# Kernel tuning notes

Measured on AMD Instinct MI355X. Metric: run time of the kernel, lower is better.

The kernel has to match this reference:

```python
import jax, jax.numpy as jnp
import numpy as np

B, E, H = 32768, 512, 512


def setup_inputs() -> dict:
    key = jax.random.key(0)
    ks = jax.random.split(key, 7)
    s_e = 1.0 / np.sqrt(E)
    s_h = 1.0 / np.sqrt(H)
    return {
        "input": jax.random.normal(ks[0], (B, E), jnp.float32),
        "h0": jax.random.normal(ks[1], (B, H), jnp.float32),
        "c0": jax.random.normal(ks[2], (B, H), jnp.float32),
        # stacked weights, gate order [i, f, o, g]
        "W_x": jax.random.uniform(ks[3], (4, H, E), jnp.float32, -s_e, s_e),
        "b_x": jax.random.uniform(ks[4], (4, H), jnp.float32, -s_e, s_e),
        "W_h": jax.random.uniform(ks[5], (4, H, H), jnp.float32, -s_h, s_h),
        "b_h": jax.random.uniform(ks[6], (4, H), jnp.float32, -s_h, s_h),
    }


def reference(input, h0, c0, W_x, b_x, W_h, b_h):
    # Fused: two GEMMs over stacked gate weights, then elementwise gate math.
    # z: [4, B, H]; gate order i, f, o, g
    z = (jnp.einsum('be,khe->kbh', input, W_x) + b_x[:, None, :]
         + jnp.einsum('bh,kgh->kbg', h0, W_h) + b_h[:, None, :])
    i = jax.nn.sigmoid(z[0])
    f = jax.nn.sigmoid(z[1])
    o = jax.nn.sigmoid(z[2])
    g = jnp.tanh(z[3])
    c1 = f * c0 + i * g
    h1 = o * jnp.tanh(c1)
    return (h1, c1)
```

## Files before the change

### kernel.cpp

```cpp
#include <hip/hip_runtime.h>
#include <hip/hip_bf16.h>


#define BQ 32768
#define HQ 512
#define KK 1024
#define BH (32768 * 512)

typedef __bf16 bf16x8 __attribute__((ext_vector_type(8)));
typedef float f32x4 __attribute__((ext_vector_type(4)));

__device__ __forceinline__ unsigned short f2bf(float f) {
    unsigned int u = __float_as_uint(f);
    unsigned int r = (u + 0x7fffu + ((u >> 16) & 1u)) >> 16;
    return (unsigned short)r;
}

__device__ __forceinline__ void gld_lds16(const unsigned short* g, unsigned short* l) {
    __builtin_amdgcn_global_load_lds(
        (const __attribute__((address_space(1))) void*)g,
        (__attribute__((address_space(3))) void*)l,
        16, 0, 0);
}


__global__ __launch_bounds__(256) void pack_X(const float* __restrict__ in,
                                              const float* __restrict__ h0,
                                              unsigned short* __restrict__ Xcat) {
    const int NQ = BQ * HQ / 4;
    int gi = blockIdx.x * 256 + threadIdx.x;
    const float* src;
    size_t dst;
    if (gi < NQ) {
        int e = gi * 4;
        int b = e >> 9, col = e & 511;
        src = in + e;
        dst = (size_t)b * 1024 + col;
    } else {
        int e = (gi - NQ) * 4;
        int b = e >> 9, col = e & 511;
        src = h0 + e;
        dst = (size_t)b * 1024 + 512 + col;
    }
    float4 v = *(const float4*)src;
    ushort4 o;
    o.x = f2bf(v.x); o.y = f2bf(v.y); o.z = f2bf(v.z); o.w = f2bf(v.w);
    *(ushort4*)&Xcat[dst] = o;
}

__global__ __launch_bounds__(256) void pack_W(const float* __restrict__ Wx,
                                              const float* __restrict__ Wh,
                                              const float* __restrict__ bx,
                                              const float* __restrict__ bh,
                                              unsigned short* __restrict__ Wint,
                                              float* __restrict__ biasc) {
    int j = blockIdx.x * 256 + threadIdx.x;
    int c = j >> 8;
    int kc = (j & 255) * 4;
    int gate = (c >> 4) & 3;
    int h = ((c >> 6) << 4) + (c & 15);
    const float* src = (kc < 512)
        ? (Wx + ((size_t)gate * 512 + h) * 512 + kc)
        : (Wh + ((size_t)gate * 512 + h) * 512 + (kc - 512));
    float4 v = *(const float4*)src;
    ushort4 o;
    o.x = f2bf(v.x); o.y = f2bf(v.y); o.z = f2bf(v.z); o.w = f2bf(v.w);
    *(ushort4*)&Wint[(size_t)c * 1024 + kc] = o;
    if ((j & 255) == 0) biasc[c] = bx[gate * 512 + h] + bh[gate * 512 + h];
}


__global__ __launch_bounds__(256) void lstm_gemm(const unsigned short* __restrict__ Xcat,
                                                 const unsigned short* __restrict__ Wint,
                                                 const float* __restrict__ biasc,
                                                 const float* __restrict__ c0,
                                                 float* __restrict__ out) {
    __shared__ __align__(16) unsigned short ldsA[128 * 32];
    __shared__ __align__(16) unsigned short ldsB[128 * 32];

    const int tid = threadIdx.x;
    const int lane = tid & 63;
    const int wave = tid >> 6;
    const int wm = wave >> 1;
    const int wn = wave & 1;
    const int quad = lane >> 4;
    const int lrow = lane & 15;
    const int koff = quad * 8;

    const int bn = blockIdx.x;
    const int bm = blockIdx.y;
    const int m0 = bm * 128;
    const int n0 = bn * 128;

    const int arow = tid >> 2;
    const int acol = (tid & 3) * 8;

    f32x4 acc[4][4];
    for (int i = 0; i < 4; i++)
        for (int j = 0; j < 4; j++) {
            f32x4 z = {0.f, 0.f, 0.f, 0.f};
            acc[i][j] = z;
        }

    const unsigned short* gA = Xcat + (size_t)(m0 + arow) * KK + acol;
    const unsigned short* gB = Wint + (size_t)(n0 + arow) * KK + acol;

    for (int kt = 0; kt < KK; kt += 32) {
        gld_lds16(gA + kt, &ldsA[tid * 8]);
        gld_lds16(gA + (size_t)64 * KK + kt, &ldsA[2048 + tid * 8]);
        gld_lds16(gB + kt, &ldsB[tid * 8]);
        gld_lds16(gB + (size_t)64 * KK + kt, &ldsB[2048 + tid * 8]);
        __syncthreads();

        bf16x8 af[4], bfr[4];
        for (int mi = 0; mi < 4; mi++)
            af[mi] = *(const bf16x8*)&ldsA[(wm * 64 + mi * 16 + lrow) * 32 + koff];
        for (int ni = 0; ni < 4; ni++)
            bfr[ni] = *(const bf16x8*)&ldsB[(wn * 64 + ni * 16 + lrow) * 32 + koff];
        for (int mi = 0; mi < 4; mi++)
            for (int ni = 0; ni < 4; ni++)
                acc[mi][ni] = __builtin_amdgcn_mfma_f32_16x16x32_bf16(
                    af[mi], bfr[ni], acc[mi][ni], 0, 0, 0);
        __syncthreads();
    }

    float bi[4];
    for (int ni = 0; ni < 4; ni++)
        bi[ni] = biasc[n0 + wn * 64 + ni * 16 + lrow];
    const int h = (bn * 2 + wn) * 16 + lrow;

    for (int mi = 0; mi < 4; mi++) {
        for (int r = 0; r < 4; r++) {
            int b = m0 + wm * 64 + mi * 16 + quad * 4 + r;
            float zi = acc[mi][0][r] + bi[0];
            float zf = acc[mi][1][r] + bi[1];
            float zo = acc[mi][2][r] + bi[2];
            float zg = acc[mi][3][r] + bi[3];
            float ig = 1.f / (1.f + __expf(-zi));
            float fg = 1.f / (1.f + __expf(-zf));
            float og = 1.f / (1.f + __expf(-zo));
            float gg = 1.f - 2.f / (__expf(2.f * zg) + 1.f);
            float c0v = c0[(size_t)b * HQ + h];
            float c1 = fg * c0v + ig * gg;
            float th = 1.f - 2.f / (__expf(2.f * c1) + 1.f);
            out[(size_t)b * HQ + h] = og * th;
            out[(size_t)BH + (size_t)b * HQ + h] = c1;
        }
    }
}

extern "C" void kernel_launch(void* const* d_in, const int* in_sizes, int n_in,
                              void* d_out, int out_size, void* d_ws, size_t ws_size,
                              hipStream_t stream) {
    (void)in_sizes; (void)n_in; (void)out_size; (void)ws_size;
    const float* input = (const float*)d_in[0];
    const float* h0    = (const float*)d_in[1];
    const float* c0    = (const float*)d_in[2];
    const float* Wx    = (const float*)d_in[3];
    const float* bx    = (const float*)d_in[4];
    const float* Wh    = (const float*)d_in[5];
    const float* bh    = (const float*)d_in[6];
    float* out = (float*)d_out;

    char* ws = (char*)d_ws;
    unsigned short* Xcat = (unsigned short*)ws;
    unsigned short* Wint = (unsigned short*)(ws + (size_t)67108864);
    float* biasc = (float*)(ws + (size_t)71303168);

    pack_X<<<32768, 256, 0, stream>>>(input, h0, Xcat);
    pack_W<<<2048, 256, 0, stream>>>(Wx, Wh, bx, bh, Wint, biasc);
    lstm_gemm<<<dim3(16, 256), 256, 0, stream>>>(Xcat, Wint, biasc, c0, out);
}
```

Baseline: 474.2 us.

## Triple-buffer LDS pipeline with 256x128 tiles, swizzle, and block remap

The GEMM kernel now uses 512-thread blocks computing 256x128 tiles. A three-stage LDS ring buffer prefetches two K-steps ahead, using explicit vmcnt waits and raw barriers instead of __syncthreads. It also XOR-swizzles LDS columns to avoid bank conflicts, raises MFMA priority with s_setprio, and remaps block IDs for L2 locality. Together these aim to hide global-load latency and raise MFMA utilization. The cost is larger LDS use (72KB per block) and hand-tuned waitcnt values that must match the number of outstanding loads exactly.

Measured after the change: 418.9 us. -11.7%, faster.

```diff
diff --git a/kernel.cpp b/kernel.cpp
--- a/kernel.cpp
+++ b/kernel.cpp
@@ -1,5 +1,4 @@
 #include <hip/hip_runtime.h>
-#include <hip/hip_bf16.h>
 
 
 #define BQ 32768
@@ -70,13 +69,13 @@
 }
 
 
-__global__ __launch_bounds__(256) void lstm_gemm(const unsigned short* __restrict__ Xcat,
-                                                 const unsigned short* __restrict__ Wint,
-                                                 const float* __restrict__ biasc,
-                                                 const float* __restrict__ c0,
-                                                 float* __restrict__ out) {
-    __shared__ __align__(16) unsigned short ldsA[128 * 32];
-    __shared__ __align__(16) unsigned short ldsB[128 * 32];
+__global__ __launch_bounds__(512, 4) void lstm_gemm(const unsigned short* __restrict__ Xcat,
+                                                    const unsigned short* __restrict__ Wint,
+                                                    const float* __restrict__ biasc,
+                                                    const float* __restrict__ c0,
+                                                    float* __restrict__ out) {
+    __shared__ __align__(16) unsigned short ldsA[3][256 * 32];
+    __shared__ __align__(16) unsigned short ldsB[3][128 * 32];
 
     const int tid = threadIdx.x;
     const int lane = tid & 63;
@@ -85,51 +84,96 @@
     const int wn = wave & 1;
     const int quad = lane >> 4;
     const int lrow = lane & 15;
-    const int koff = quad * 8;
-
-    const int bn = blockIdx.x;
-    const int bm = blockIdx.y;
-    const int m0 = bm * 128;
+
+    const int bid = blockIdx.x;
+    const int l = bid >> 3;
+    const int bm = (bid & 7) * 16 + (l >> 4);
+    const int bn = l & 15;
+    const int m0 = bm * 256;
     const int n0 = bn * 128;
 
-    const int arow = tid >> 2;
-    const int acol = (tid & 3) * 8;
+    const int srow = tid >> 2;
+    const int scol = ((tid & 3) ^ ((tid >> 3) & 3)) * 8;
+    const unsigned short* pA  = Xcat + (size_t)(m0 + srow) * KK + scol;
+    const unsigned short* pA2 = pA + (size_t)128 * KK;
+    const unsigned short* pB  = Wint + (size_t)(n0 + srow) * KK + scol;
+
+    const int koff = (quad ^ ((lrow >> 1) & 3)) * 8;
+    const int ar = (wm * 64 + lrow) * 32 + koff;
+    const int br = (wn * 64 + lrow) * 32 + koff;
 
     f32x4 acc[4][4];
+#pragma unroll
     for (int i = 0; i < 4; i++)
+#pragma unroll
         for (int j = 0; j < 4; j++) {
             f32x4 z = {0.f, 0.f, 0.f, 0.f};
             acc[i][j] = z;
         }
 
-    const unsigned short* gA = Xcat + (size_t)(m0 + arow) * KK + acol;
-    const unsigned short* gB = Wint + (size_t)(n0 + arow) * KK + acol;
-
-    for (int kt = 0; kt < KK; kt += 32) {
-        gld_lds16(gA + kt, &ldsA[tid * 8]);
-        gld_lds16(gA + (size_t)64 * KK + kt, &ldsA[2048 + tid * 8]);
-        gld_lds16(gB + kt, &ldsB[tid * 8]);
-        gld_lds16(gB + (size_t)64 * KK + kt, &ldsB[2048 + tid * 8]);
-        __syncthreads();
-
-        bf16x8 af[4], bfr[4];
-        for (int mi = 0; mi < 4; mi++)
-            af[mi] = *(const bf16x8*)&ldsA[(wm * 64 + mi * 16 + lrow) * 32 + koff];
-        for (int ni = 0; ni < 4; ni++)
-            bfr[ni] = *(const bf16x8*)&ldsB[(wn * 64 + ni * 16 + lrow) * 32 + koff];
-        for (int mi = 0; mi < 4; mi++)
-            for (int ni = 0; ni < 4; ni++)
-                acc[mi][ni] = __builtin_amdgcn_mfma_f32_16x16x32_bf16(
-                    af[mi], bfr[ni], acc[mi][ni], 0, 0, 0);
-        __syncthreads();
+#define STAGE(Tt, W) do { const int ko_ = (Tt) * 32;                           \
+    gld_lds16(pA  + ko_, &ldsA[W][tid * 8]);                                   \
+    gld_lds16(pA2 + ko_, &ldsA[W][4096 + tid * 8]);                            \
+    gld_lds16(pB  + ko_, &ldsB[W][tid * 8]);                                   \
+} while (0)
+
+#define COMPUTE(R) do {                                                        \
+    bf16x8 af[4], bfr[4];                                                      \
+    _Pragma("unroll")                                                          \
+    for (int mi = 0; mi < 4; mi++)                                             \
+        af[mi] = *(const bf16x8*)&ldsA[R][ar + mi * 512];                      \
+    _Pragma("unroll")                                                          \
+    for (int g = 0; g < 4; g++)                                                \
+        bfr[g] = *(const bf16x8*)&ldsB[R][br + g * 512];                       \
+    __builtin_amdgcn_s_setprio(1);                                             \
+    _Pragma("unroll")                                                          \
+    for (int mi = 0; mi < 4; mi++)                                             \
+        _Pragma("unroll")                                                      \
+        for (int g = 0; g < 4; g++)                                            \
+            acc[mi][g] = __builtin_amdgcn_mfma_f32_16x16x32_bf16(              \
+                af[mi], bfr[g], acc[mi][g], 0, 0, 0);                          \
+    __builtin_amdgcn_s_setprio(0);                                             \
+} while (0)
+
+#define ITER(Tt, R, W) do {                                                    \
+    STAGE((Tt) + 2, W);                                                        \
+    asm volatile("s_waitcnt vmcnt(6)" ::: "memory");                           \
+    __builtin_amdgcn_s_barrier();                                              \
+    __builtin_amdgcn_sched_barrier(0);                                         \
+    COMPUTE(R);                                                                \
+    __builtin_amdgcn_s_barrier();                                              \
+} while (0)
+
+    STAGE(0, 0);
+    STAGE(1, 1);
+
+    for (int T = 0; T < 30; T += 3) {
+        ITER(T + 0, 0, 2);
+        ITER(T + 1, 1, 0);
+        ITER(T + 2, 2, 1);
     }
+    asm volatile("s_waitcnt vmcnt(3)" ::: "memory");
+    __builtin_amdgcn_s_barrier();
+    __builtin_amdgcn_sched_barrier(0);
+    COMPUTE(0);
+    asm volatile("s_waitcnt vmcnt(0)" ::: "memory");
+    __builtin_amdgcn_s_barrier();
+    __builtin_amdgcn_sched_barrier(0);
+    COMPUTE(1);
+
+#undef ITER
+#undef COMPUTE
+#undef STAGE
 
     float bi[4];
-    for (int ni = 0; ni < 4; ni++)
-        bi[ni] = biasc[n0 + wn * 64 + ni * 16 + lrow];
+#pragma unroll
+    for (int g = 0; g < 4; g++)
+        bi[g] = biasc[n0 + wn * 64 + g * 16 + lrow];
     const int h = (bn * 2 + wn) * 16 + lrow;
 
+#pragma unroll
     for (int mi = 0; mi < 4; mi++) {
+#pragma unroll
         for (int r = 0; r < 4; r++) {
             int b = m0 + wm * 64 + mi * 16 + quad * 4 + r;
             float zi = acc[mi][0][r] + bi[0];
@@ -169,5 +213,5 @@
 
     pack_X<<<32768, 256, 0, stream>>>(input, h0, Xcat);
     pack_W<<<2048, 256, 0, stream>>>(Wx, Wh, bx, bh, Wint, biasc);
-    lstm_gemm<<<dim3(16, 256), 256, 0, stream>>>(Xcat, Wint, biasc, c0, out);
-}
+    lstm_gemm<<<2048, 512, 0, stream>>>(Xcat, Wint, biasc, c0, out);
+}
```

## Keep full-K weight tile resident in LDS and stream A directly from global

Applied to the files above, without the earlier changes.

The GEMM kernel now uses 512-thread blocks that load a 64-column by full-K weight slab (128 KB) into swizzled LDS once. Each wave streams its A rows straight from global memory into registers with a two-stage prefetch, so the per-k-step barriers are gone. Block indices are remapped to group M tiles for L2 reuse. The trade-offs are heavy LDS use, which limits occupancy, and A reads that bypass LDS sharing, so A is fetched from memory once per N block.

Measured after the change: 614.3 us. +29.5%, slower.

```diff
diff --git a/kernel.cpp b/kernel.cpp
--- a/kernel.cpp
+++ b/kernel.cpp
@@ -1,5 +1,4 @@
 #include <hip/hip_runtime.h>
-#include <hip/hip_bf16.h>
 
 
 #define BQ 32768
@@ -70,68 +69,112 @@
 }
 
 
-__global__ __launch_bounds__(256) void lstm_gemm(const unsigned short* __restrict__ Xcat,
-                                                 const unsigned short* __restrict__ Wint,
-                                                 const float* __restrict__ biasc,
-                                                 const float* __restrict__ c0,
-                                                 float* __restrict__ out) {
-    __shared__ __align__(16) unsigned short ldsA[128 * 32];
-    __shared__ __align__(16) unsigned short ldsB[128 * 32];
+__global__ __launch_bounds__(512, 2) void lstm_gemm(const unsigned short* __restrict__ Xcat,
+                                                    const unsigned short* __restrict__ Wint,
+                                                    const float* __restrict__ biasc,
+                                                    const float* __restrict__ c0,
+                                                    float* __restrict__ out) {
+    __shared__ __align__(16) unsigned short ldsB[32 * 2048];
 
     const int tid = threadIdx.x;
     const int lane = tid & 63;
     const int wave = tid >> 6;
-    const int wm = wave >> 1;
-    const int wn = wave & 1;
     const int quad = lane >> 4;
     const int lrow = lane & 15;
-    const int koff = quad * 8;
-
-    const int bn = blockIdx.x;
-    const int bm = blockIdx.y;
-    const int m0 = bm * 128;
-    const int n0 = bn * 128;
-
-    const int arow = tid >> 2;
-    const int acol = (tid & 3) * 8;
+
+    const int bid = blockIdx.x;
+    const int bm = (bid & 7) + ((bid >> 8) << 3);
+    const int bn = (bid >> 3) & 31;
+    const int m0 = bm * 512;
+    const int n0r = bn * 64;
+
+#pragma unroll
+    for (int j = 0; j < 16; ++j) {
+        const int s = j * 8 + wave;
+        const int row = ((s & 3) << 4) + (lane >> 2);
+        const int col = ((s >> 2) << 5) + (((lane & 3) ^ ((lane >> 3) & 3)) << 3);
+        gld_lds16(Wint + (size_t)(n0r + row) * KK + col, &ldsB[s * 512 + lane * 8]);
+    }
+    __syncthreads();
+
+    const unsigned short* gA0 = Xcat + (size_t)(m0 + wave * 64 +  0 + lrow) * KK + quad * 8;
+    const unsigned short* gA1 = Xcat + (size_t)(m0 + wave * 64 + 16 + lrow) * KK + quad * 8;
+    const unsigned short* gA2 = Xcat + (size_t)(m0 + wave * 64 + 32 + lrow) * KK + quad * 8;
+    const unsigned short* gA3 = Xcat + (size_t)(m0 + wave * 64 + 48 + lrow) * KK + quad * 8;
+
+    const int koff = (quad ^ ((lrow >> 1) & 3)) * 8;
+    const int br0 = (0 * 16 + lrow) * 32 + koff;
+    const int br1 = (1 * 16 + lrow) * 32 + koff;
+    const int br2 = (2 * 16 + lrow) * 32 + koff;
+    const int br3 = (3 * 16 + lrow) * 32 + koff;
 
     f32x4 acc[4][4];
+#pragma unroll
     for (int i = 0; i < 4; i++)
+#pragma unroll
         for (int j = 0; j < 4; j++) {
             f32x4 z = {0.f, 0.f, 0.f, 0.f};
             acc[i][j] = z;
         }
 
-    const unsigned short* gA = Xcat + (size_t)(m0 + arow) * KK + acol;
-    const unsigned short* gB = Wint + (size_t)(n0 + arow) * KK + acol;
-
-    for (int kt = 0; kt < KK; kt += 32) {
-        gld_lds16(gA + kt, &ldsA[tid * 8]);
-        gld_lds16(gA + (size_t)64 * KK + kt, &ldsA[2048 + tid * 8]);
-        gld_lds16(gB + kt, &ldsB[tid * 8]);
-        gld_lds16(gB + (size_t)64 * KK + kt, &ldsB[2048 + tid * 8]);
-        __syncthreads();
-
-        bf16x8 af[4], bfr[4];
-        for (int mi = 0; mi < 4; mi++)
-            af[mi] = *(const bf16x8*)&ldsA[(wm * 64 + mi * 16 + lrow) * 32 + koff];
-        for (int ni = 0; ni < 4; ni++)
-            bfr[ni] = *(const bf16x8*)&ldsB[(wn * 64 + ni * 16 + lrow) * 32 + koff];
-        for (int mi = 0; mi < 4; mi++)
-            for (int ni = 0; ni < 4; ni++)
-                acc[mi][ni] = __builtin_amdgcn_mfma_f32_16x16x32_bf16(
-                    af[mi], bfr[ni], acc[mi][ni], 0, 0, 0);
-        __syncthreads();
-    }
+    bf16x8 preA0 = *(const bf16x8*)(gA0);
+    bf16x8 preA1 = *(const bf16x8*)(gA1);
+    bf16x8 preA2 = *(const bf16x8*)(gA2);
+    bf16x8 preA3 = *(const bf16x8*)(gA3);
+    bf16x8 preB0 = *(const bf16x8*)(gA0 + 32);
+    bf16x8 preB1 = *(const bf16x8*)(gA1 + 32);
+    bf16x8 preB2 = *(const bf16x8*)(gA2 + 32);
+    bf16x8 preB3 = *(const bf16x8*)(gA3 + 32);
+
+#define BODY(T, P) do {                                                        \
+    bf16x8 a0 = pre##P##0, a1 = pre##P##1, a2 = pre##P##2, a3 = pre##P##3;     \
+    if ((T) < 30) {                                                            \
+        pre##P##0 = *(const bf16x8*)(gA0 + ((T) + 2) * 32);                    \
+        pre##P##1 = *(const bf16x8*)(gA1 + ((T) + 2) * 32);                    \
+        pre##P##2 = *(const bf16x8*)(gA2 + ((T) + 2) * 32);                    \
+        pre##P##3 = *(const bf16x8*)(gA3 + ((T) + 2) * 32);                    \
+    }                                                                          \
+    const int tb_ = (T) * 2048;                                                \
+    bf16x8 b0 = *(const bf16x8*)&ldsB[tb_ + br0];                              \
+    bf16x8 b1 = *(const bf16x8*)&ldsB[tb_ + br1];                              \
+    bf16x8 b2 = *(const bf16x8*)&ldsB[tb_ + br2];                              \
+    bf16x8 b3 = *(const bf16x8*)&ldsB[tb_ + br3];                              \
+    acc[0][0] = __builtin_amdgcn_mfma_f32_16x16x32_bf16(a0, b0, acc[0][0], 0, 0, 0); \
+    acc[1][0] = __builtin_amdgcn_mfma_f32_16x16x32_bf16(a1, b0, acc[1][0], 0, 0, 0); \
+    acc[2][0] = __builtin_amdgcn_mfma_f32_16x16x32_bf16(a2, b0, acc[2][0], 0, 0, 0); \
+    acc[3][0] = __builtin_amdgcn_mfma_f32_16x16x32_bf16(a3, b0, acc[3][0], 0, 0, 0); \
+    acc[0][1] = __builtin_amdgcn_mfma_f32_16x16x32_bf16(a0, b1, acc[0][1], 0, 0, 0); \
+    acc[1][1] = __builtin_amdgcn_mfma_f32_16x16x32_bf16(a1, b1, acc[1][1], 0, 0, 0); \
+    acc[2][1] = __builtin_amdgcn_mfma_f32_16x16x32_bf16(a2, b1, acc[2][1], 0, 0, 0); \
+    acc[3][1] = __builtin_amdgcn_mfma_f32_16x16x32_bf16(a3, b1, acc[3][1], 0, 0, 0); \
+    acc[0][2] = __builtin_amdgcn_mfma_f32_16x16x32_bf16(a0, b2, acc[0][2], 0, 0, 0); \
+    acc[1][2] = __builtin_amdgcn_mfma_f32_16x16x32_bf16(a1, b2, acc[1][2], 0, 0, 0); \
+    acc[2][2] = __builtin_amdgcn_mfma_f32_16x16x32_bf16(a2, b2, acc[2][2], 0, 0, 0); \
+    acc[3][2] = __builtin_amdgcn_mfma_f32_16x16x32_bf16(a3, b2, acc[3][2], 0, 0, 0); \
+    acc[0][3] = __builtin_amdgcn_mfma_f32_16x16x32_bf16(a0, b3, acc[0][3], 0, 0, 0); \
+    acc[1][3] = __builtin_amdgcn_mfma_f32_16x16x32_bf16(a1, b3, acc[1][3], 0, 0, 0); \
+    acc[2][3] = __builtin_amdgcn_mfma_f32_16x16x32_bf16(a2, b3, acc[2][3], 0, 0, 0); \
+    acc[3][3] = __builtin_amdgcn_mfma_f32_16x16x32_bf16(a3, b3, acc[3][3], 0, 0, 0); \
+} while (0)
+
+#pragma unroll
+    for (int TT = 0; TT < 16; ++TT) {
+        BODY(2 * TT, A);
+        BODY(2 * TT + 1, B);
+    }
+#undef BODY
 
     float bi[4];
-    for (int ni = 0; ni < 4; ni++)
-        bi[ni] = biasc[n0 + wn * 64 + ni * 16 + lrow];
-    const int h = (bn * 2 + wn) * 16 + lrow;
-
+#pragma unroll
+    for (int g = 0; g < 4; g++)
+        bi[g] = biasc[n0r + g * 16 + lrow];
+    const int h = bn * 16 + lrow;
+
+#pragma unroll
     for (int mi = 0; mi < 4; mi++) {
+#pragma unroll
         for (int r = 0; r < 4; r++) {
-            int b = m0 + wm * 64 + mi * 16 + quad * 4 + r;
+            int b = m0 + wave * 64 + mi * 16 + quad * 4 + r;
             float zi = acc[mi][0][r] + bi[0];
             float zf = acc[mi][1][r] + bi[1];
             float zo = acc[mi][2][r] + bi[2];
@@ -169,5 +212,5 @@
 
     pack_X<<<32768, 256, 0, stream>>>(input, h0, Xcat);
     pack_W<<<2048, 256, 0, stream>>>(Wx, Wh, bx, bh, Wint, biasc);
-    lstm_gemm<<<dim3(16, 256), 256, 0, stream>>>(Xcat, Wint, biasc, c0, out);
-}
+    lstm_gemm<<<2048, 512, 0, stream>>>(Xcat, Wint, biasc, c0, out);
+}
```
